# Performance work log

Measured on AMD Instinct MI355X. Metric: run time of the kernel, lower is better.

## Reference

```python
import jax, jax.numpy as jnp
import numpy as np

SEPS = 1e-6
LEPS = 1e6
NUM_MAIN_SEQ_ATOMS = 12
K = 30          # num_atom_neighbours
EMB_DIM = 128   # atom_embedding_dim
B, N = 2, 4800  # batch, num_atoms (= max_len * NUM_MAIN_SEQ_ATOMS)


def setup_inputs() -> dict:
    key = jax.random.key(0)
    k1, k2 = jax.random.split(key)
    atom_coords = jax.random.normal(k1, (B, N, 3), dtype=jnp.float32) * 10.0
    atom_mask = jnp.ones((B, N), dtype=jnp.float32)
    emb_weight = jax.random.normal(k2, (NUM_MAIN_SEQ_ATOMS, EMB_DIM), dtype=jnp.float32)
    scale = jnp.ones((1, 1, EMB_DIM), dtype=jnp.float32)
    shift = jnp.zeros((1, 1, EMB_DIM), dtype=jnp.float32)
    return {"atom_coords": atom_coords, "atom_mask": atom_mask,
            "emb_weight": emb_weight, "scale": scale, "shift": shift}


def _graph_norm(features, mask, scale, shift):
    # features: (B,N,D), mask: (B,N)
    m = mask[..., None]                                   # (B,N,1)
    mf = features * m
    cnt = jnp.sum(m, axis=1, keepdims=True)               # (B,1,1)
    cnt = jnp.where(cnt == 0, 1.0, cnt)
    mean = jnp.sum(mf, axis=1, keepdims=True) / cnt       # (B,1,D)
    var = jnp.sum((mf - mean) ** 2, axis=1, keepdims=True) / cnt
    std = jnp.sqrt(var + SEPS)
    out = (features - mean) / std * scale + shift
    return out * m


def reference(atom_coords, atom_mask, emb_weight, scale, shift):
    Bv, Nv, _ = atom_coords.shape
    # ---- atom embedding (cyclic atom types) + graph norm ----
    atom_types = jnp.arange(Nv) % NUM_MAIN_SEQ_ATOMS       # (N,)
    emb = emb_weight[atom_types]                           # (N,D)
    emb = jnp.broadcast_to(emb[None], (Bv, Nv, EMB_DIM)) * atom_mask[..., None]
    atom_embedding = _graph_norm(emb, atom_mask, scale, shift)

    # ---- kNN graph over pairwise distances ----
    d = atom_coords[:, None, :, :] - atom_coords[:, :, None, :]  # (B,N,N,3)
    distances = jnp.sqrt(jnp.sum(d * d, axis=-1) + SEPS)         # (B,N,N)
    distances = distances + jnp.eye(Nv, dtype=distances.dtype)[None] * LEPS
    mask2d = atom_mask[:, None, :] * atom_mask[:, :, None]       # (B,N,N)
    distances = distances * mask2d + (1.0 - mask2d) * LEPS

    neg_dists, edge_idx = jax.lax.top_k(-distances, K)           # smallest-k
    cross_dists = -neg_dists                                     # (B,N,K)

    node_indices = jnp.arange(Nv).reshape(1, -1, 1)
    edge_idx = jnp.where(edge_idx == node_indices, -1, edge_idx)
    pad = (atom_mask == 0)[..., None]                            # (B,N,1)
    edge_idx = jnp.where(pad, -1, edge_idx)
    cross_dists = jnp.where(pad, LEPS, cross_dists)
    return atom_embedding, cross_dists, edge_idx
```

## Files before the change

### kernel.cpp

```cpp
#include <hip/hip_runtime.h>
#include <stdint.h>

#define NTYPES 12
#define EMB 128
#define KNN 30
#define SEPS_F 1e-6f
#define LEPS_F 1e6f
#define NATOMS 4800
#define GROUPS 19
#define PADN 4864
#define CAPH 64
#define ROWS_PB 4
#define SENT16 0x7F7Fu

typedef unsigned long long ull;
typedef float f32x2 __attribute__((ext_vector_type(2)));
typedef float f32x4 __attribute__((ext_vector_type(4)));

__device__ __forceinline__ ull shfl_xor64(ull v, int m) {
    int lo = (int)(unsigned)(v & 0xffffffffull);
    int hi = (int)(unsigned)(v >> 32);
    lo = __shfl_xor(lo, m, 64);
    hi = __shfl_xor(hi, m, 64);
    return ((ull)(unsigned)hi << 32) | (unsigned)lo;
}

__device__ __forceinline__ f32x2 pk_add(f32x2 a, f32x2 b) {
    f32x2 d; asm("v_pk_add_f32 %0, %1, %2" : "=v"(d) : "v"(a), "v"(b)); return d;
}
__device__ __forceinline__ f32x2 pk_mul(f32x2 a, f32x2 b) {
    f32x2 d; asm("v_pk_mul_f32 %0, %1, %2" : "=v"(d) : "v"(a), "v"(b)); return d;
}
__device__ __forceinline__ f32x2 pk_fma(f32x2 a, f32x2 b, f32x2 c) {
    f32x2 d; asm("v_pk_fma_f32 %0, %1, %2, %3" : "=v"(d) : "v"(a), "v"(b), "v"(c)); return d;
}
__device__ __forceinline__ unsigned pk_min_u16(unsigned a, unsigned b) {
    unsigned d; asm("v_pk_min_u16 %0, %1, %2" : "=v"(d) : "v"(a), "v"(b)); return d;
}

__device__ __forceinline__ f32x2 d2pk(f32x2 x, f32x2 y, f32x2 z,
                                      f32x2 nqx, f32x2 nqy, f32x2 nqz) {
    f32x2 dx = pk_add(x, nqx), dy = pk_add(y, nqy), dz = pk_add(z, nqz);
    return pk_fma(dx, dx, pk_fma(dy, dy, pk_mul(dz, dz)));
}

__device__ __forceinline__ unsigned bu(f32x2 v) {
    return __builtin_amdgcn_perm(__float_as_uint(v.y), __float_as_uint(v.x),
                                 0x07060302u);
}

__device__ __forceinline__ unsigned d2x(float x, float y, float z,
                                        float qx, float qy, float qz) {
    float dx = __fsub_rn(x, qx), dy = __fsub_rn(y, qy), dz = __fsub_rn(z, qz);
    float d2 = __fadd_rn(__fadd_rn(__fmul_rn(dx, dx), __fmul_rn(dy, dy)),
                         __fmul_rn(dz, dz));
    return __float_as_uint(d2);
}

__global__ __launch_bounds__(256) void prep_soa_kernel(const float* __restrict__ mask,
                                                       const float* __restrict__ w,
                                                       const float* __restrict__ scale,
                                                       const float* __restrict__ shift,
                                                       const float* __restrict__ coords,
                                                       float* __restrict__ cnt_all,
                                                       float* __restrict__ Aa,
                                                       float* __restrict__ Bb,
                                                       float* __restrict__ soa,
                                                       int B, int N) {
    if ((int)blockIdx.x < B) {
        __shared__ float lc[NTYPES];
        __shared__ float ltot;
        const int b = blockIdx.x;
        const int t = threadIdx.x;
        if (t < NTYPES) lc[t] = 0.f;
        if (t == 0) ltot = 0.f;
        __syncthreads();
        float s0 = 0.f, s1 = 0.f, s2 = 0.f, tot = 0.f;
        const float* mb = mask + (size_t)b * N;
#pragma unroll
        for (int base = 0; base < 21; base += 3) {
            int n0 = t + 256 * base;
            if (n0 < N) { float m = mb[n0]; s0 += m; tot += m; }
            int n1 = t + 256 * (base + 1);
            if (n1 < N) { float m = mb[n1]; s1 += m; tot += m; }
            int n2 = t + 256 * (base + 2);
            if (n2 < N) { float m = mb[n2]; s2 += m; tot += m; }
        }
        atomicAdd(&lc[t % NTYPES], s0);
        atomicAdd(&lc[(t + 4) % NTYPES], s1);
        atomicAdd(&lc[(t + 8) % NTYPES], s2);
        for (int s = 32; s >= 1; s >>= 1) tot += __shfl_xor(tot, s, 64);
        if ((t & 63) == 0) atomicAdd(&ltot, tot);
        __syncthreads();
        if (t < EMB) {
            const int d = t;
            float cnt = ltot;
            float c = (cnt == 0.f) ? 1.f : cnt;
            float mean = 0.f;
#pragma unroll
            for (int tt = 0; tt < NTYPES; ++tt) mean += w[tt * EMB + d] * lc[tt];
            mean /= c;
            float S = 0.f;
#pragma unroll
            for (int tt = 0; tt < NTYPES; ++tt) {
                float dv = w[tt * EMB + d] - mean;
                S += lc[tt] * dv * dv;
            }
            S += ((float)N - cnt) * mean * mean;
            float stdv = sqrtf(S / c + SEPS_F);
            float g = scale[d] / stdv;
            Aa[b * EMB + d] = g;
            Bb[b * EMB + d] = shift[d] - mean * g;
        }
        if (t == 0) cnt_all[b] = ltot;
    } else {
        int idx = blockIdx.x - B;
        const int b = idx / GROUPS;
        const int chunk = idx % GROUPS;
        const int j = chunk * 256 + threadIdx.x;
        float x, y, z;
        int slot;
        if (j < N) {
            int t = j >> 6, l = j & 63;
            slot = (t >> 2) * 256 + l * 4 + (t & 3);
            const float* cp = coords + ((size_t)b * N + j) * 3;
            x = cp[0]; y = cp[1]; z = cp[2];
        } else {
            int l = j - N;
            slot = (GROUPS - 1) * 256 + l * 4 + 3;
            x = y = z = 1.0e30f;
        }
        float* base = soa + (size_t)b * 3 * PADN;
        base[0 * PADN + slot] = x;
        base[1 * PADN + slot] = y;
        base[2 * PADN + slot] = z;
    }
}

__global__ __launch_bounds__(256) void knn_kernel(const float* __restrict__ coords,
                                                  const float* __restrict__ soa,
                                                  const float* __restrict__ mask,
                                                  const float* __restrict__ cnt_all,
                                                  const float* __restrict__ w,
                                                  const float* __restrict__ Aa,
                                                  const float* __restrict__ Bb,
                                                  float* __restrict__ out0,
                                                  float* __restrict__ outd,
                                                  float* __restrict__ outi,
                                                  int B, int N) {
    __shared__ unsigned short lmx[ROWS_PB][2][64];
    __shared__ unsigned candj[ROWS_PB][2][CAPH];
    __shared__ int cnts[ROWS_PB][2];

    const int wv = threadIdx.x >> 6;
    const int lane = threadIdx.x & 63;
    const int pr = wv >> 1;
    const int h = wv & 1;
    const int r0 = blockIdx.x * ROWS_PB;
    const int b = r0 / N;
    const int iA = (r0 + 2 * pr) - b * N;
    const int iB = iA + 1;

    const float* cb = coords + (size_t)b * N * 3;
    const float* mb = mask + (size_t)b * N;
    const bool allOnes = (cnt_all[b] == (float)N);

    const float qxA = cb[iA * 3], qyA = cb[iA * 3 + 1], qzA = cb[iA * 3 + 2];
    const float qxB = cb[iB * 3], qyB = cb[iB * 3 + 1], qzB = cb[iB * 3 + 2];
    const f32x2 nqxA = {-qxA, -qxA}, nqyA = {-qyA, -qyA}, nqzA = {-qzA, -qzA};
    const f32x2 nqxB = {-qxB, -qxB}, nqyB = {-qyB, -qyB}, nqzB = {-qzB, -qzB};

    const float* xs = soa + (size_t)b * 3 * PADN;
    const float* ys = xs + PADN;
    const float* zs = ys + PADN;
    const int loff = lane << 2;
    const int gbase = h ? 10 : 0;
    const int tbase = 4 * gbase;

    unsigned pkA[20], pkB[20];
    unsigned lmA2 = 0xFFFFFFFFu, lmB2 = 0xFFFFFFFFu;

#define PROC_GROUP(P, S0, S1)                                                     \
    {                                                                             \
        const int g = gbase + (P);                                                \
        const f32x4 xv = *(const f32x4*)(xs + g * 256 + loff);                    \
        const f32x4 yv = *(const f32x4*)(ys + g * 256 + loff);                    \
        const f32x4 zv = *(const f32x4*)(zs + g * 256 + loff);                    \
        const f32x2 xlo = {xv.x, xv.y}, xhi = {xv.z, xv.w};                       \
        const f32x2 ylo = {yv.x, yv.y}, yhi = {yv.z, yv.w};                       \
        const f32x2 zlo = {zv.x, zv.y}, zhi = {zv.z, zv.w};                       \
        unsigned a01 = bu(d2pk(xlo, ylo, zlo, nqxA, nqyA, nqzA));                 \
        unsigned a23 = bu(d2pk(xhi, yhi, zhi, nqxA, nqyA, nqzA));                 \
        unsigned b01 = bu(d2pk(xlo, ylo, zlo, nqxB, nqyB, nqzB));                 \
        unsigned b23 = bu(d2pk(xhi, yhi, zhi, nqxB, nqyB, nqzB));                 \
        if (!allOnes) {                                                           \
            const int t0 = 4 * g;                                                 \
            int j0 = (t0 + 0) * 64 + lane;                                        \
            int j1 = (t0 + 1) * 64 + lane;                                        \
            int j2 = (t0 + 2) * 64 + lane;                                        \
            int j3 = (t0 + 3) * 64 + lane;                                        \
            if (j0 < N && mb[j0] == 0.f) { a01 = (a01 & 0xFFFF0000u) | SENT16;    \
                                           b01 = (b01 & 0xFFFF0000u) | SENT16; }  \
            if (j1 < N && mb[j1] == 0.f) { a01 = (a01 & 0xFFFFu) | (SENT16 << 16);\
                                           b01 = (b01 & 0xFFFFu) | (SENT16 << 16);}\
            if (j2 < N && mb[j2] == 0.f) { a23 = (a23 & 0xFFFF0000u) | SENT16;    \
                                           b23 = (b23 & 0xFFFF0000u) | SENT16; }  \
            if (j3 < N && mb[j3] == 0.f) { a23 = (a23 & 0xFFFFu) | (SENT16 << 16);\
                                           b23 = (b23 & 0xFFFFu) | (SENT16 << 16);}\
        }                                                                         \
        lmA2 = pk_min_u16(pk_min_u16(lmA2, a01), a23);                            \
        lmB2 = pk_min_u16(pk_min_u16(lmB2, b01), b23);                            \
        pkA[S0] = a01; pkA[S1] = a23;                                             \
        pkB[S0] = b01; pkB[S1] = b23;                                             \
    }

    PROC_GROUP(0, 0, 1)   PROC_GROUP(1, 2, 3)   PROC_GROUP(2, 4, 5)
    PROC_GROUP(3, 6, 7)   PROC_GROUP(4, 8, 9)   PROC_GROUP(5, 10, 11)
    PROC_GROUP(6, 12, 13) PROC_GROUP(7, 14, 15) PROC_GROUP(8, 16, 17)
    if (h == 0) {
        PROC_GROUP(9, 18, 19)
    } else {
        pkA[18] = pkA[19] = 0xFFFFFFFFu;
        pkB[18] = pkB[19] = 0xFFFFFFFFu;
    }
#undef PROC_GROUP

    unsigned lmA16 = lmA2 & 0xFFFFu; { unsigned t2 = lmA2 >> 16; if (t2 < lmA16) lmA16 = t2; }
    unsigned lmB16 = lmB2 & 0xFFFFu; { unsigned t2 = lmB2 >> 16; if (t2 < lmB16) lmB16 = t2; }
    lmx[2 * pr][h][lane] = (unsigned short)lmA16;
    lmx[2 * pr + 1][h][lane] = (unsigned short)lmB16;
    __syncthreads();
    const unsigned ptA = lmx[2 * pr][h ^ 1][lane];
    const unsigned ptB = lmx[2 * pr + 1][h ^ 1][lane];

    unsigned loA = 0, hiA = 0x7F80u, loB = 0, hiB = 0x7F80u;
    for (int it = 0; it < 15; ++it) {
        unsigned mA = (loA + hiA) >> 1, mB = (loB + hiB) >> 1;
        int cA = __popcll(__ballot(lmA16 <= mA)) + __popcll(__ballot(ptA <= mA));
        int cB = __popcll(__ballot(lmB16 <= mB)) + __popcll(__ballot(ptB <= mB));
        if (cA >= 31) hiA = mA; else loA = mA + 1;
        if (cB >= 31) hiB = mB; else loB = mB + 1;
    }
    const unsigned TsA = hiA + 2, TsB = hiB + 2;

    const ull lmaskLT = (1ull << lane) - 1ull;
    {
        unsigned* dst = candj[2 * pr][h];
        int c = 0;
#pragma unroll
        for (int p = 0; p < 20; ++p) {
            unsigned reg = pkA[p];
            bool pe = (reg & 0xFFFFu) <= TsA;
            ull be = __ballot(pe);
            if (pe) {
                int pos = c + __popcll(be & lmaskLT);
                if (pos < CAPH) dst[pos] = (unsigned)((tbase + 2 * p) * 64 + lane);
            }
            c += __popcll(be);
            bool po = (reg >> 16) <= TsA;
            ull bo = __ballot(po);
            if (po) {
                int pos = c + __popcll(bo & lmaskLT);
                if (pos < CAPH) dst[pos] = (unsigned)((tbase + 2 * p + 1) * 64 + lane);
            }
            c += __popcll(bo);
        }
        if (lane == 0) cnts[2 * pr][h] = (c > CAPH) ? CAPH : c;
    }
    {
        unsigned* dst = candj[2 * pr + 1][h];
        int c = 0;
#pragma unroll
        for (int p = 0; p < 20; ++p) {
            unsigned reg = pkB[p];
            bool pe = (reg & 0xFFFFu) <= TsB;
            ull be = __ballot(pe);
            if (pe) {
                int pos = c + __popcll(be & lmaskLT);
                if (pos < CAPH) dst[pos] = (unsigned)((tbase + 2 * p) * 64 + lane);
            }
            c += __popcll(be);
            bool po = (reg >> 16) <= TsB;
            ull bo = __ballot(po);
            if (po) {
                int pos = c + __popcll(bo & lmaskLT);
                if (pos < CAPH) dst[pos] = (unsigned)((tbase + 2 * p + 1) * 64 + lane);
            }
            c += __popcll(bo);
        }
        if (lane == 0) cnts[2 * pr + 1][h] = (c > CAPH) ? CAPH : c;
    }
    __syncthreads();

    const int lr = wv;
    const int row = r0 + lr;
    const int i = row - b * N;
    const float mi = mb[i];

    {
        const int d0 = lane * 2;
        const float2 wvv = *(const float2*)(w + (i % NTYPES) * EMB + d0);
        const float2 av = *(const float2*)(Aa + b * EMB + d0);
        const float2 bv2 = *(const float2*)(Bb + b * EMB + d0);
        float2 o;
        o.x = (wvv.x * mi * av.x + bv2.x) * mi;
        o.y = (wvv.y * mi * av.y + bv2.y) * mi;
        *(float2*)(out0 + ((size_t)b * N + i) * EMB + d0) = o;
    }

    if (mi == 0.f) {
        if (lane < KNN) {
            size_t o0 = (size_t)row * KNN + lane;
            outd[o0] = LEPS_F;
            outi[o0] = -1.f;
        }
        return;
    }

    const int c0 = cnts[lr][0];
    const int ct = c0 + cnts[lr][1];
    const float qx = cb[i * 3], qy = cb[i * 3 + 1], qz = cb[i * 3 + 2];

    auto makeKey = [&](int ci) -> ull {
        unsigned j = (ci < c0) ? candj[lr][0][ci] : candj[lr][1][ci - c0];
        if (j >= (unsigned)N) return ~0ull;
        const float* cj = cb + (size_t)j * 3;
        float mj = allOnes ? 1.f : mb[j];
        unsigned db = d2x(cj[0], cj[1], cj[2], qx, qy, qz);
        float dist = (j == (unsigned)i || mj == 0.f)
                         ? LEPS_F
                         : __fsqrt_rn(__fadd_rn(__uint_as_float(db), SEPS_F));
        return ((ull)__float_as_uint(dist) << 32) | j;
    };

    ull k0 = (lane < ct) ? makeKey(lane) : ~0ull;

    if (ct <= 64) {
#pragma unroll
        for (int kk = 2; kk <= 64; kk <<= 1) {
            for (int jj = kk >> 1; jj > 0; jj >>= 1) {
                ull o = shfl_xor64(k0, jj);
                bool tm = (((lane & jj) == 0) == ((lane & kk) == 0));
                ull mn = (k0 < o) ? k0 : o;
                ull mv = (k0 < o) ? o : k0;
                k0 = tm ? mn : mv;
            }
        }
    } else {
        ull k1 = (lane + 64 < ct) ? makeKey(lane + 64) : ~0ull;
#pragma unroll
        for (int kk = 2; kk <= 32; kk <<= 1) {
            for (int jj = kk >> 1; jj > 0; jj >>= 1) {
                bool tm = (((lane & jj) == 0) == ((lane & kk) == 0));
                ull o0 = shfl_xor64(k0, jj);
                k0 = tm ? ((k0 < o0) ? k0 : o0) : ((k0 < o0) ? o0 : k0);
                ull o1 = shfl_xor64(k1, jj);
                k1 = tm ? ((k1 < o1) ? k1 : o1) : ((k1 < o1) ? o1 : k1);
            }
        }
        for (int jj = 32; jj > 0; jj >>= 1) {
            bool up = ((lane & jj) == 0);
            ull o0 = shfl_xor64(k0, jj);
            k0 = up ? ((k0 < o0) ? k0 : o0) : ((k0 < o0) ? o0 : k0);
            ull o1 = shfl_xor64(k1, jj);
            k1 = (!up) ? ((k1 < o1) ? k1 : o1) : ((k1 < o1) ? o1 : k1);
        }
        {
            ull mn = (k0 < k1) ? k0 : k1;
            ull mv = (k0 < k1) ? k1 : k0;
            k0 = mn; k1 = mv;
        }
        for (int jj = 32; jj > 0; jj >>= 1) {
            bool tm = ((lane & jj) == 0);
            ull o0 = shfl_xor64(k0, jj);
            k0 = tm ? ((k0 < o0) ? k0 : o0) : ((k0 < o0) ? o0 : k0);
            ull o1 = shfl_xor64(k1, jj);
            k1 = tm ? ((k1 < o1) ? k1 : o1) : ((k1 < o1) ? o1 : k1);
        }
    }

    if (lane < KNN) {
        unsigned db = (unsigned)(k0 >> 32);
        unsigned jj = (unsigned)k0;
        size_t o0 = (size_t)row * KNN + lane;
        outd[o0] = __uint_as_float(db);
        outi[o0] = (jj == (unsigned)i) ? -1.f : (float)jj;
    }
}

extern "C" void kernel_launch(void* const* d_in, const int* in_sizes, int n_in,
                              void* d_out, int out_size, void* d_ws, size_t ws_size,
                              hipStream_t stream) {
    const float* coords = (const float*)d_in[0];
    const float* mask   = (const float*)d_in[1];
    const float* w      = (const float*)d_in[2];
    const float* scale  = (const float*)d_in[3];
    const float* shift  = (const float*)d_in[4];

    int BN = in_sizes[1];
    int N  = NATOMS;
    int B  = BN / N;

    float* ws0     = (float*)d_ws;
    float* cnt_all = ws0;
    float* Aa      = ws0 + 16;
    float* Bb      = Aa + B * EMB;
    float* soa     = Bb + B * EMB;

    float* out0 = (float*)d_out;
    float* outd = out0 + (size_t)B * N * EMB;
    float* outi = outd + (size_t)B * N * KNN;

    prep_soa_kernel<<<B + B * GROUPS, 256, 0, stream>>>(mask, w, scale, shift, coords,
                                                        cnt_all, Aa, Bb, soa, B, N);
    knn_kernel<<<(B * N) / ROWS_PB, 256, 0, stream>>>(coords, soa, mask, cnt_all,
                                                      w, Aa, Bb, out0, outd, outi, B, N);
}
```

Before: 38.50 us.

## Split candidate scan across four waves, each covering all four rows

The old kernel had each pair of waves split the atoms in half for two query rows. Now each of the four waves scans a quarter of the atom groups for all four rows of the block, so each coordinate load is reused across four queries instead of two. Per-wave minima are shared through LDS, and one wave per row runs the threshold bisection. The candidate lists are then merged from four segments of capacity 32. This reduces redundant global/L2 loads but adds more registers (pk[4][10]), an extra barrier, and a tighter per-segment capacity that could truncate candidates if they cluster.

```diff
diff --git a/kernel.cpp b/kernel.cpp
--- a/kernel.cpp
+++ b/kernel.cpp
@@ -9,8 +9,7 @@
 #define NATOMS 4800
 #define GROUPS 19
 #define PADN 4864
-#define CAPH 64
-#define ROWS_PB 4
+#define CAPQ 32
 #define SENT16 0x7F7Fu
 
 typedef unsigned long long ull;
@@ -148,156 +147,24 @@
                                                   float* __restrict__ outd,
                                                   float* __restrict__ outi,
                                                   int B, int N) {
-    __shared__ unsigned short lmx[ROWS_PB][2][64];
-    __shared__ unsigned candj[ROWS_PB][2][CAPH];
-    __shared__ int cnts[ROWS_PB][2];
-
-    const int wv = threadIdx.x >> 6;
+    __shared__ unsigned short lmx[4][64][4];
+    __shared__ unsigned candj[4][4][CAPQ];
+    __shared__ int cnts[4][4];
+    __shared__ unsigned tselS[4];
+
+    const int qtr = threadIdx.x >> 6;
     const int lane = threadIdx.x & 63;
-    const int pr = wv >> 1;
-    const int h = wv & 1;
-    const int r0 = blockIdx.x * ROWS_PB;
+    const int r0 = blockIdx.x * 4;
     const int b = r0 / N;
-    const int iA = (r0 + 2 * pr) - b * N;
-    const int iB = iA + 1;
+    const int i0 = r0 - b * N;
 
     const float* cb = coords + (size_t)b * N * 3;
     const float* mb = mask + (size_t)b * N;
     const bool allOnes = (cnt_all[b] == (float)N);
 
-    const float qxA = cb[iA * 3], qyA = cb[iA * 3 + 1], qzA = cb[iA * 3 + 2];
-    const float qxB = cb[iB * 3], qyB = cb[iB * 3 + 1], qzB = cb[iB * 3 + 2];
-    const f32x2 nqxA = {-qxA, -qxA}, nqyA = {-qyA, -qyA}, nqzA = {-qzA, -qzA};
-    const f32x2 nqxB = {-qxB, -qxB}, nqyB = {-qyB, -qyB}, nqzB = {-qzB, -qzB};
-
-    const float* xs = soa + (size_t)b * 3 * PADN;
-    const float* ys = xs + PADN;
-    const float* zs = ys + PADN;
-    const int loff = lane << 2;
-    const int gbase = h ? 10 : 0;
-    const int tbase = 4 * gbase;
-
-    unsigned pkA[20], pkB[20];
-    unsigned lmA2 = 0xFFFFFFFFu, lmB2 = 0xFFFFFFFFu;
-
-#define PROC_GROUP(P, S0, S1)                                                     \
-    {                                                                             \
-        const int g = gbase + (P);                                                \
-        const f32x4 xv = *(const f32x4*)(xs + g * 256 + loff);                    \
-        const f32x4 yv = *(const f32x4*)(ys + g * 256 + loff);                    \
-        const f32x4 zv = *(const f32x4*)(zs + g * 256 + loff);                    \
-        const f32x2 xlo = {xv.x, xv.y}, xhi = {xv.z, xv.w};                       \
-        const f32x2 ylo = {yv.x, yv.y}, yhi = {yv.z, yv.w};                       \
-        const f32x2 zlo = {zv.x, zv.y}, zhi = {zv.z, zv.w};                       \
-        unsigned a01 = bu(d2pk(xlo, ylo, zlo, nqxA, nqyA, nqzA));                 \
-        unsigned a23 = bu(d2pk(xhi, yhi, zhi, nqxA, nqyA, nqzA));                 \
-        unsigned b01 = bu(d2pk(xlo, ylo, zlo, nqxB, nqyB, nqzB));                 \
-        unsigned b23 = bu(d2pk(xhi, yhi, zhi, nqxB, nqyB, nqzB));                 \
-        if (!allOnes) {                                                           \
-            const int t0 = 4 * g;                                                 \
-            int j0 = (t0 + 0) * 64 + lane;                                        \
-            int j1 = (t0 + 1) * 64 + lane;                                        \
-            int j2 = (t0 + 2) * 64 + lane;                                        \
-            int j3 = (t0 + 3) * 64 + lane;                                        \
-            if (j0 < N && mb[j0] == 0.f) { a01 = (a01 & 0xFFFF0000u) | SENT16;    \
-                                           b01 = (b01 & 0xFFFF0000u) | SENT16; }  \
-            if (j1 < N && mb[j1] == 0.f) { a01 = (a01 & 0xFFFFu) | (SENT16 << 16);\
-                                           b01 = (b01 & 0xFFFFu) | (SENT16 << 16);}\
-            if (j2 < N && mb[j2] == 0.f) { a23 = (a23 & 0xFFFF0000u) | SENT16;    \
-                                           b23 = (b23 & 0xFFFF0000u) | SENT16; }  \
-            if (j3 < N && mb[j3] == 0.f) { a23 = (a23 & 0xFFFFu) | (SENT16 << 16);\
-                                           b23 = (b23 & 0xFFFFu) | (SENT16 << 16);}\
-        }                                                                         \
-        lmA2 = pk_min_u16(pk_min_u16(lmA2, a01), a23);                            \
-        lmB2 = pk_min_u16(pk_min_u16(lmB2, b01), b23);                            \
-        pkA[S0] = a01; pkA[S1] = a23;                                             \
-        pkB[S0] = b01; pkB[S1] = b23;                                             \
-    }
-
-    PROC_GROUP(0, 0, 1)   PROC_GROUP(1, 2, 3)   PROC_GROUP(2, 4, 5)
-    PROC_GROUP(3, 6, 7)   PROC_GROUP(4, 8, 9)   PROC_GROUP(5, 10, 11)
-    PROC_GROUP(6, 12, 13) PROC_GROUP(7, 14, 15) PROC_GROUP(8, 16, 17)
-    if (h == 0) {
-        PROC_GROUP(9, 18, 19)
-    } else {
-        pkA[18] = pkA[19] = 0xFFFFFFFFu;
-        pkB[18] = pkB[19] = 0xFFFFFFFFu;
-    }
-#undef PROC_GROUP
-
-    unsigned lmA16 = lmA2 & 0xFFFFu; { unsigned t2 = lmA2 >> 16; if (t2 < lmA16) lmA16 = t2; }
-    unsigned lmB16 = lmB2 & 0xFFFFu; { unsigned t2 = lmB2 >> 16; if (t2 < lmB16) lmB16 = t2; }
-    lmx[2 * pr][h][lane] = (unsigned short)lmA16;
-    lmx[2 * pr + 1][h][lane] = (unsigned short)lmB16;
-    __syncthreads();
-    const unsigned ptA = lmx[2 * pr][h ^ 1][lane];
-    const unsigned ptB = lmx[2 * pr + 1][h ^ 1][lane];
-
-    unsigned loA = 0, hiA = 0x7F80u, loB = 0, hiB = 0x7F80u;
-    for (int it = 0; it < 15; ++it) {
-        unsigned mA = (loA + hiA) >> 1, mB = (loB + hiB) >> 1;
-        int cA = __popcll(__ballot(lmA16 <= mA)) + __popcll(__ballot(ptA <= mA));
-        int cB = __popcll(__ballot(lmB16 <= mB)) + __popcll(__ballot(ptB <= mB));
-        if (cA >= 31) hiA = mA; else loA = mA + 1;
-        if (cB >= 31) hiB = mB; else loB = mB + 1;
-    }
-    const unsigned TsA = hiA + 2, TsB = hiB + 2;
-
-    const ull lmaskLT = (1ull << lane) - 1ull;
     {
-        unsigned* dst = candj[2 * pr][h];
-        int c = 0;
-#pragma unroll
-        for (int p = 0; p < 20; ++p) {
-            unsigned reg = pkA[p];
-            bool pe = (reg & 0xFFFFu) <= TsA;
-            ull be = __ballot(pe);
-            if (pe) {
-                int pos = c + __popcll(be & lmaskLT);
-                if (pos < CAPH) dst[pos] = (unsigned)((tbase + 2 * p) * 64 + lane);
-            }
-            c += __popcll(be);
-            bool po = (reg >> 16) <= TsA;
-            ull bo = __ballot(po);
-            if (po) {
-                int pos = c + __popcll(bo & lmaskLT);
-                if (pos < CAPH) dst[pos] = (unsigned)((tbase + 2 * p + 1) * 64 + lane);
-            }
-            c += __popcll(bo);
-        }
-        if (lane == 0) cnts[2 * pr][h] = (c > CAPH) ? CAPH : c;
-    }
-    {
-        unsigned* dst = candj[2 * pr + 1][h];
-        int c = 0;
-#pragma unroll
-        for (int p = 0; p < 20; ++p) {
-            unsigned reg = pkB[p];
-            bool pe = (reg & 0xFFFFu) <= TsB;
-            ull be = __ballot(pe);
-            if (pe) {
-                int pos = c + __popcll(be & lmaskLT);
-                if (pos < CAPH) dst[pos] = (unsigned)((tbase + 2 * p) * 64 + lane);
-            }
-            c += __popcll(be);
-            bool po = (reg >> 16) <= TsB;
-            ull bo = __ballot(po);
-            if (po) {
-                int pos = c + __popcll(bo & lmaskLT);
-                if (pos < CAPH) dst[pos] = (unsigned)((tbase + 2 * p + 1) * 64 + lane);
-            }
-            c += __popcll(bo);
-        }
-        if (lane == 0) cnts[2 * pr + 1][h] = (c > CAPH) ? CAPH : c;
-    }
-    __syncthreads();
-
-    const int lr = wv;
-    const int row = r0 + lr;
-    const int i = row - b * N;
-    const float mi = mb[i];
-
-    {
+        const int i = i0 + qtr;
+        const float mi = mb[i];
         const int d0 = lane * 2;
         const float2 wvv = *(const float2*)(w + (i % NTYPES) * EMB + d0);
         const float2 av = *(const float2*)(Aa + b * EMB + d0);
@@ -308,6 +175,113 @@
         *(float2*)(out0 + ((size_t)b * N + i) * EMB + d0) = o;
     }
 
+    f32x2 nqx[4], nqy[4], nqz[4];
+#pragma unroll
+    for (int r = 0; r < 4; ++r) {
+        float qxr = cb[(i0 + r) * 3], qyr = cb[(i0 + r) * 3 + 1], qzr = cb[(i0 + r) * 3 + 2];
+        nqx[r] = {-qxr, -qxr}; nqy[r] = {-qyr, -qyr}; nqz[r] = {-qzr, -qzr};
+    }
+
+    const float* xs = soa + (size_t)b * 3 * PADN;
+    const float* ys = xs + PADN;
+    const float* zs = ys + PADN;
+    const int loff = lane << 2;
+
+    unsigned pk[4][10];
+    unsigned lm2[4] = {~0u, ~0u, ~0u, ~0u};
+#pragma unroll
+    for (int p = 0; p < 5; ++p) {
+        const int g = qtr + 4 * p;
+        if (g < GROUPS) {
+            const f32x4 xv = *(const f32x4*)(xs + g * 256 + loff);
+            const f32x4 yv = *(const f32x4*)(ys + g * 256 + loff);
+            const f32x4 zv = *(const f32x4*)(zs + g * 256 + loff);
+            const f32x2 xlo = {xv.x, xv.y}, xhi = {xv.z, xv.w};
+            const f32x2 ylo = {yv.x, yv.y}, yhi = {yv.z, yv.w};
+            const f32x2 zlo = {zv.x, zv.y}, zhi = {zv.z, zv.w};
+            unsigned msk = 0;
+            if (!allOnes) {
+                const int t0 = 4 * g;
+                if (mb[(t0 + 0) * 64 + lane] == 0.f) msk |= 1;
+                if (mb[(t0 + 1) * 64 + lane] == 0.f) msk |= 2;
+                if (mb[(t0 + 2) * 64 + lane] == 0.f) msk |= 4;
+                if (g != GROUPS - 1 && mb[(t0 + 3) * 64 + lane] == 0.f) msk |= 8;
+            }
+#pragma unroll
+            for (int r = 0; r < 4; ++r) {
+                unsigned a01 = bu(d2pk(xlo, ylo, zlo, nqx[r], nqy[r], nqz[r]));
+                unsigned a23 = bu(d2pk(xhi, yhi, zhi, nqx[r], nqy[r], nqz[r]));
+                if (msk & 1) a01 = (a01 & 0xFFFF0000u) | SENT16;
+                if (msk & 2) a01 = (a01 & 0xFFFFu) | (SENT16 << 16);
+                if (msk & 4) a23 = (a23 & 0xFFFF0000u) | SENT16;
+                if (msk & 8) a23 = (a23 & 0xFFFFu) | (SENT16 << 16);
+                lm2[r] = pk_min_u16(pk_min_u16(lm2[r], a01), a23);
+                pk[r][2 * p] = a01;
+                pk[r][2 * p + 1] = a23;
+            }
+        } else {
+#pragma unroll
+            for (int r = 0; r < 4; ++r) { pk[r][2 * p] = ~0u; pk[r][2 * p + 1] = ~0u; }
+        }
+    }
+
+#pragma unroll
+    for (int r = 0; r < 4; ++r) {
+        unsigned a = lm2[r] & 0xFFFFu, bq = lm2[r] >> 16;
+        lmx[r][lane][qtr] = (unsigned short)((a < bq) ? a : bq);
+    }
+    __syncthreads();
+
+    {
+        ull mv = *(const ull*)&lmx[qtr][lane][0];
+        unsigned m0 = (unsigned)(mv & 0xFFFFu);
+        unsigned m1 = (unsigned)((mv >> 16) & 0xFFFFu);
+        unsigned m2 = (unsigned)((mv >> 32) & 0xFFFFu);
+        unsigned m3 = (unsigned)(mv >> 48);
+        unsigned lo = 0, hi = 0x7F80u;
+        for (int it = 0; it < 15; ++it) {
+            unsigned mid = (lo + hi) >> 1;
+            int cnt = __popcll(__ballot(m0 <= mid)) + __popcll(__ballot(m1 <= mid)) +
+                      __popcll(__ballot(m2 <= mid)) + __popcll(__ballot(m3 <= mid));
+            if (cnt >= 31) hi = mid; else lo = mid + 1;
+        }
+        if (lane == 0) tselS[qtr] = hi + 2;
+    }
+    __syncthreads();
+
+    const ull lmaskLT = (1ull << lane) - 1ull;
+#pragma unroll
+    for (int r = 0; r < 4; ++r) {
+        const unsigned T = tselS[r];
+        unsigned* dst = candj[r][qtr];
+        int c = 0;
+#pragma unroll
+        for (int s = 0; s < 10; ++s) {
+            unsigned reg = pk[r][s];
+            const int tI = 4 * (qtr + 4 * (s >> 1)) + 2 * (s & 1);
+            bool pe = (reg & 0xFFFFu) <= T;
+            ull be = __ballot(pe);
+            if (pe) {
+                int pos = c + __popcll(be & lmaskLT);
+                if (pos < CAPQ) dst[pos] = (unsigned)(tI * 64 + lane);
+            }
+            c += __popcll(be);
+            bool po = (reg >> 16) <= T;
+            ull bo = __ballot(po);
+            if (po) {
+                int pos = c + __popcll(bo & lmaskLT);
+                if (pos < CAPQ) dst[pos] = (unsigned)((tI + 1) * 64 + lane);
+            }
+            c += __popcll(bo);
+        }
+        if (lane == 0) cnts[r][qtr] = (c > CAPQ) ? CAPQ : c;
+    }
+    __syncthreads();
+
+    const int i = i0 + qtr;
+    const int row = r0 + qtr;
+    const float mi = mb[i];
+
     if (mi == 0.f) {
         if (lane < KNN) {
             size_t o0 = (size_t)row * KNN + lane;
@@ -317,12 +291,18 @@
         return;
     }
 
-    const int c0 = cnts[lr][0];
-    const int ct = c0 + cnts[lr][1];
+    const int o1 = cnts[qtr][0];
+    const int o2 = o1 + cnts[qtr][1];
+    const int o3 = o2 + cnts[qtr][2];
+    const int ct = o3 + cnts[qtr][3];
     const float qx = cb[i * 3], qy = cb[i * 3 + 1], qz = cb[i * 3 + 2];
 
     auto makeKey = [&](int ci) -> ull {
-        unsigned j = (ci < c0) ? candj[lr][0][ci] : candj[lr][1][ci - c0];
+        unsigned j;
+        if (ci < o1) j = candj[qtr][0][ci];
+        else if (ci < o2) j = candj[qtr][1][ci - o1];
+        else if (ci < o3) j = candj[qtr][2][ci - o2];
+        else j = candj[qtr][3][ci - o3];
         if (j >= (unsigned)N) return ~0ull;
         const float* cj = cb + (size_t)j * 3;
         float mj = allOnes ? 1.f : mb[j];
@@ -354,16 +334,16 @@
                 bool tm = (((lane & jj) == 0) == ((lane & kk) == 0));
                 ull o0 = shfl_xor64(k0, jj);
                 k0 = tm ? ((k0 < o0) ? k0 : o0) : ((k0 < o0) ? o0 : k0);
-                ull o1 = shfl_xor64(k1, jj);
-                k1 = tm ? ((k1 < o1) ? k1 : o1) : ((k1 < o1) ? o1 : k1);
+                ull o1x = shfl_xor64(k1, jj);
+                k1 = tm ? ((k1 < o1x) ? k1 : o1x) : ((k1 < o1x) ? o1x : k1);
             }
         }
         for (int jj = 32; jj > 0; jj >>= 1) {
             bool up = ((lane & jj) == 0);
             ull o0 = shfl_xor64(k0, jj);
             k0 = up ? ((k0 < o0) ? k0 : o0) : ((k0 < o0) ? o0 : k0);
-            ull o1 = shfl_xor64(k1, jj);
-            k1 = (!up) ? ((k1 < o1) ? k1 : o1) : ((k1 < o1) ? o1 : k1);
+            ull o1x = shfl_xor64(k1, jj);
+            k1 = (!up) ? ((k1 < o1x) ? k1 : o1x) : ((k1 < o1x) ? o1x : k1);
         }
         {
             ull mn = (k0 < k1) ? k0 : k1;
@@ -374,8 +354,8 @@
             bool tm = ((lane & jj) == 0);
             ull o0 = shfl_xor64(k0, jj);
             k0 = tm ? ((k0 < o0) ? k0 : o0) : ((k0 < o0) ? o0 : k0);
-            ull o1 = shfl_xor64(k1, jj);
-            k1 = tm ? ((k1 < o1) ? k1 : o1) : ((k1 < o1) ? o1 : k1);
+            ull o1x = shfl_xor64(k1, jj);
+            k1 = tm ? ((k1 < o1x) ? k1 : o1x) : ((k1 < o1x) ? o1x : k1);
         }
     }
 
@@ -413,6 +393,6 @@
 
     prep_soa_kernel<<<B + B * GROUPS, 256, 0, stream>>>(mask, w, scale, shift, coords,
                                                         cnt_all, Aa, Bb, soa, B, N);
-    knn_kernel<<<(B * N) / ROWS_PB, 256, 0, stream>>>(coords, soa, mask, cnt_all,
-                                                      w, Aa, Bb, out0, outd, outi, B, N);
-}
+    knn_kernel<<<(B * N) / 4, 256, 0, stream>>>(coords, soa, mask, cnt_all,
+                                                w, Aa, Bb, out0, outd, outi, B, N);
+}
```

New measurement: 40.72 us. +5.8%, slower.
